# Kernel optimization log

Measured on AMD Instinct MI355X. Metric: run time of the kernel, lower is better.

The kernel has to match this reference:

```python
import jax, jax.numpy as jnp
import numpy as np

B, S, D = 4, 4096, 64

def setup_inputs() -> dict:
    key = jax.random.key(0)
    kq, kk, kv = jax.random.split(key, 3)
    q = jax.random.normal(kq, (B, S, D), dtype=jnp.float32)
    k = jax.random.normal(kk, (B, S, D), dtype=jnp.float32)
    v = jax.random.normal(kv, (B, S, D), dtype=jnp.float32)
    return {"q": q, "k": k, "v": v}

def reference(q, k, v):
    # unnormalized attention: scores [b,i,j], then weighted sum over j
    attn = jnp.einsum('bid,bjd->bij', q, k)
    out = jnp.einsum('bij,bjd->bid', attn, v)
    return out
```

## Files before the change

kernel.cpp:

```cpp
#include <hip/hip_runtime.h>
#include <hip/hip_bf16.h>


#define BATCH 4
#define SEQ   4096
#define DIM   64
#define NCH   64
#define CHUNK 64

typedef float f4  __attribute__((ext_vector_type(4)));
typedef short bf16x8 __attribute__((ext_vector_type(8)));
typedef float f32x4  __attribute__((ext_vector_type(4)));

__device__ inline unsigned short f2bf(float f) {
    union { float f; unsigned u; } v; v.f = f;
    unsigned r = (v.u + 0x7fffu + ((v.u >> 16) & 1u)) >> 16;
    return (unsigned short)r;
}

__global__ __launch_bounds__(256) void k1_partial(const float* __restrict__ K,
                                                  const float* __restrict__ V,
                                                  float* __restrict__ part) {
    __shared__ f4 Ks[1024];
    __shared__ f4 Vs[1024];
    const int bx = blockIdx.x;
    const int t  = threadIdx.x;
    const f4* Kg = (const f4*)(K + (size_t)bx * (CHUNK * DIM));
    const f4* Vg = (const f4*)(V + (size_t)bx * (CHUNK * DIM));
#pragma unroll
    for (int i = 0; i < 4; ++i) {
        Ks[t + 256 * i] = Kg[t + 256 * i];
        Vs[t + 256 * i] = Vg[t + 256 * i];
    }
    __syncthreads();
    const int rg = t >> 4;
    const int cg = t & 15;
    f4 acc0 = 0.f, acc1 = 0.f, acc2 = 0.f, acc3 = 0.f;
#pragma unroll 8
    for (int j = 0; j < CHUNK; ++j) {
        f4 a = Ks[j * 16 + rg];
        f4 v = Vs[j * 16 + cg];
        acc0 += v * a.x;
        acc1 += v * a.y;
        acc2 += v * a.z;
        acc3 += v * a.w;
    }
    f4* P = (f4*)part + (size_t)bx * 1024;
    P[(rg * 4 + 0) * 16 + cg] = acc0;
    P[(rg * 4 + 1) * 16 + cg] = acc1;
    P[(rg * 4 + 2) * 16 + cg] = acc2;
    P[(rg * 4 + 3) * 16 + cg] = acc3;
}

__global__ __launch_bounds__(256) void k2_reduce(const float* __restrict__ part,
                                                 unsigned short* __restrict__ MB) {
    const int tg = blockIdx.x * 256 + threadIdx.x;
    const int b = tg >> 12;
    const int e = tg & 4095;
    float s = 0.f;
#pragma unroll 8
    for (int p = 0; p < NCH; ++p)
        s += part[((size_t)(b * NCH + p)) * 4096 + e];
    const int dp = e >> 6;
    const int c  = e & 63;
    const int ct = c >> 4, m = c & 15;
    const int ks = dp >> 5, quad = (dp >> 3) & 3, j = dp & 7;
    const int idx = (((b * 8 + ct * 2 + ks) * 64) + quad * 16 + m) * 8 + j;
    MB[idx] = f2bf(s);
}

__global__ __launch_bounds__(256) void k3_qm(const float* __restrict__ Q,
                                             const unsigned short* __restrict__ MB,
                                             float* __restrict__ out) {
    const int bx = blockIdx.x;
    const int t  = threadIdx.x;
    const int wave = t >> 6, lane = t & 63;
    const int m = lane & 15, quad = lane >> 4;
    const int b = bx >> 6;
    const int row0 = (bx & 63) * 64 + wave * 16;

    const float* qrow = Q + ((size_t)b * SEQ + row0 + m) * DIM;
    bf16x8 afrag[2];
#pragma unroll
    for (int ks = 0; ks < 2; ++ks) {
        const f4* qp = (const f4*)(qrow + ks * 32 + quad * 8);
        f4 q1 = qp[0], q2 = qp[1];
        bf16x8 a;
        a[0] = (short)f2bf(q1.x); a[1] = (short)f2bf(q1.y);
        a[2] = (short)f2bf(q1.z); a[3] = (short)f2bf(q1.w);
        a[4] = (short)f2bf(q2.x); a[5] = (short)f2bf(q2.y);
        a[6] = (short)f2bf(q2.z); a[7] = (short)f2bf(q2.w);
        afrag[ks] = a;
    }

    const bf16x8* MBv = (const bf16x8*)MB + (size_t)b * 8 * 64;
    f32x4 acc[4];
#pragma unroll
    for (int ct = 0; ct < 4; ++ct) { acc[ct] = (f32x4)0.f; }
#pragma unroll
    for (int ct = 0; ct < 4; ++ct) {
#pragma unroll
        for (int ks = 0; ks < 2; ++ks) {
            bf16x8 bfrag = MBv[(ct * 2 + ks) * 64 + lane];
            acc[ct] = __builtin_amdgcn_mfma_f32_16x16x32_bf16(afrag[ks], bfrag, acc[ct], 0, 0, 0);
        }
    }

    float* orow = out + ((size_t)b * SEQ + row0) * DIM;
#pragma unroll
    for (int ct = 0; ct < 4; ++ct) {
#pragma unroll
        for (int r = 0; r < 4; ++r) {
            orow[(quad * 4 + r) * DIM + ct * 16 + m] = acc[ct][r];
        }
    }
}

extern "C" void kernel_launch(void* const* d_in, const int* in_sizes, int n_in,
                              void* d_out, int out_size, void* d_ws, size_t ws_size,
                              hipStream_t stream) {
    const float* q = (const float*)d_in[0];
    const float* k = (const float*)d_in[1];
    const float* v = (const float*)d_in[2];
    float* out = (float*)d_out;

    float* part = (float*)d_ws;
    unsigned short* MB = (unsigned short*)((char*)d_ws + (size_t)4 * 1024 * 1024);

    k1_partial<<<BATCH * NCH, 256, 0, stream>>>(k, v, part);
    k2_reduce<<<64, 256, 0, stream>>>(part, MB);
    k3_qm<<<BATCH * NCH, 256, 0, stream>>>(q, MB, out);
}
```

Baseline: 74.46 us.

## Fuse three kernels into one cooperative kernel with grid-wide syncs

Replaces the three separate launches (partial K^T V, reduction, Q·M MFMA) with a single cooperative kernel that uses grid.sync between stages. This is meant to remove two kernel launch gaps and their drain/fill overhead. In exchange it adds the cost of two grid-wide barriers and threadfences, and it relies on the 256 blocks being co-resident for the cooperative launch to succeed.

```diff
diff --git a/kernel.cpp b/kernel.cpp
--- a/kernel.cpp
+++ b/kernel.cpp
@@ -1,12 +1,15 @@
 #include <hip/hip_runtime.h>
 #include <hip/hip_bf16.h>
+#include <hip/hip_cooperative_groups.h>
+
+namespace cg = cooperative_groups;
 
 
 #define BATCH 4
 #define SEQ   4096
 #define DIM   64
+#define CHUNK 64
 #define NCH   64
-#define CHUNK 64
 
 typedef float f4  __attribute__((ext_vector_type(4)));
 typedef short bf16x8 __attribute__((ext_vector_type(8)));
@@ -18,101 +21,103 @@
     return (unsigned short)r;
 }
 
-__global__ __launch_bounds__(256) void k1_partial(const float* __restrict__ K,
-                                                  const float* __restrict__ V,
-                                                  float* __restrict__ part) {
+__global__ __launch_bounds__(256) void kfused(const float* __restrict__ Q,
+                                              const float* __restrict__ K,
+                                              const float* __restrict__ V,
+                                              float* __restrict__ out,
+                                              float* __restrict__ part,
+                                              unsigned short* __restrict__ MB) {
+    cg::grid_group grid = cg::this_grid();
     __shared__ f4 Ks[1024];
     __shared__ f4 Vs[1024];
     const int bx = blockIdx.x;
     const int t  = threadIdx.x;
-    const f4* Kg = (const f4*)(K + (size_t)bx * (CHUNK * DIM));
-    const f4* Vg = (const f4*)(V + (size_t)bx * (CHUNK * DIM));
+
+    {
+        const f4* Kg = (const f4*)(K + (size_t)bx * (CHUNK * DIM));
+        const f4* Vg = (const f4*)(V + (size_t)bx * (CHUNK * DIM));
 #pragma unroll
-    for (int i = 0; i < 4; ++i) {
-        Ks[t + 256 * i] = Kg[t + 256 * i];
-        Vs[t + 256 * i] = Vg[t + 256 * i];
+        for (int i = 0; i < 4; ++i) {
+            Ks[t + 256 * i] = Kg[t + 256 * i];
+            Vs[t + 256 * i] = Vg[t + 256 * i];
+        }
+        __syncthreads();
+        const int rg = t >> 4;
+        const int cg_ = t & 15;
+        f4 a0 = 0.f, a1 = 0.f, a2 = 0.f, a3 = 0.f;
+#pragma unroll 8
+        for (int j = 0; j < CHUNK; ++j) {
+            f4 a = Ks[j * 16 + rg];
+            f4 v = Vs[j * 16 + cg_];
+            a0 += v * a.x;
+            a1 += v * a.y;
+            a2 += v * a.z;
+            a3 += v * a.w;
+        }
+        f4* P = (f4*)part + (size_t)bx * 1024;
+        P[(rg * 4 + 0) * 16 + cg_] = a0;
+        P[(rg * 4 + 1) * 16 + cg_] = a1;
+        P[(rg * 4 + 2) * 16 + cg_] = a2;
+        P[(rg * 4 + 3) * 16 + cg_] = a3;
     }
-    __syncthreads();
-    const int rg = t >> 4;
-    const int cg = t & 15;
-    f4 acc0 = 0.f, acc1 = 0.f, acc2 = 0.f, acc3 = 0.f;
+    __threadfence();
+    grid.sync();
+
+    if (bx < 64) {
+        const int tg = bx * 256 + t;
+        const int b = tg >> 12;
+        const int e = tg & 4095;
+        float s = 0.f;
 #pragma unroll 8
-    for (int j = 0; j < CHUNK; ++j) {
-        f4 a = Ks[j * 16 + rg];
-        f4 v = Vs[j * 16 + cg];
-        acc0 += v * a.x;
-        acc1 += v * a.y;
-        acc2 += v * a.z;
-        acc3 += v * a.w;
+        for (int p = 0; p < NCH; ++p)
+            s += part[((size_t)(b * NCH + p)) * 4096 + e];
+        const int dp = e >> 6;
+        const int c  = e & 63;
+        const int ct = c >> 4, m = c & 15;
+        const int ks = dp >> 5, quad = (dp >> 3) & 3, j = dp & 7;
+        MB[(((b * 8 + ct * 2 + ks) * 64) + quad * 16 + m) * 8 + j] = f2bf(s);
     }
-    f4* P = (f4*)part + (size_t)bx * 1024;
-    P[(rg * 4 + 0) * 16 + cg] = acc0;
-    P[(rg * 4 + 1) * 16 + cg] = acc1;
-    P[(rg * 4 + 2) * 16 + cg] = acc2;
-    P[(rg * 4 + 3) * 16 + cg] = acc3;
-}
+    __threadfence();
+    grid.sync();
 
-__global__ __launch_bounds__(256) void k2_reduce(const float* __restrict__ part,
-                                                 unsigned short* __restrict__ MB) {
-    const int tg = blockIdx.x * 256 + threadIdx.x;
-    const int b = tg >> 12;
-    const int e = tg & 4095;
-    float s = 0.f;
-#pragma unroll 8
-    for (int p = 0; p < NCH; ++p)
-        s += part[((size_t)(b * NCH + p)) * 4096 + e];
-    const int dp = e >> 6;
-    const int c  = e & 63;
-    const int ct = c >> 4, m = c & 15;
-    const int ks = dp >> 5, quad = (dp >> 3) & 3, j = dp & 7;
-    const int idx = (((b * 8 + ct * 2 + ks) * 64) + quad * 16 + m) * 8 + j;
-    MB[idx] = f2bf(s);
-}
+    {
+        const int wave = t >> 6, lane = t & 63;
+        const int m = lane & 15, quad = lane >> 4;
+        const int b = bx >> 6;
+        const int row0 = (bx & 63) * 64 + wave * 16;
 
-__global__ __launch_bounds__(256) void k3_qm(const float* __restrict__ Q,
-                                             const unsigned short* __restrict__ MB,
-                                             float* __restrict__ out) {
-    const int bx = blockIdx.x;
-    const int t  = threadIdx.x;
-    const int wave = t >> 6, lane = t & 63;
-    const int m = lane & 15, quad = lane >> 4;
-    const int b = bx >> 6;
-    const int row0 = (bx & 63) * 64 + wave * 16;
-
-    const float* qrow = Q + ((size_t)b * SEQ + row0 + m) * DIM;
-    bf16x8 afrag[2];
-#pragma unroll
-    for (int ks = 0; ks < 2; ++ks) {
-        const f4* qp = (const f4*)(qrow + ks * 32 + quad * 8);
-        f4 q1 = qp[0], q2 = qp[1];
-        bf16x8 a;
-        a[0] = (short)f2bf(q1.x); a[1] = (short)f2bf(q1.y);
-        a[2] = (short)f2bf(q1.z); a[3] = (short)f2bf(q1.w);
-        a[4] = (short)f2bf(q2.x); a[5] = (short)f2bf(q2.y);
-        a[6] = (short)f2bf(q2.z); a[7] = (short)f2bf(q2.w);
-        afrag[ks] = a;
-    }
-
-    const bf16x8* MBv = (const bf16x8*)MB + (size_t)b * 8 * 64;
-    f32x4 acc[4];
-#pragma unroll
-    for (int ct = 0; ct < 4; ++ct) { acc[ct] = (f32x4)0.f; }
-#pragma unroll
-    for (int ct = 0; ct < 4; ++ct) {
+        const float* qrow = Q + ((size_t)b * SEQ + row0 + m) * DIM;
+        bf16x8 afrag[2];
 #pragma unroll
         for (int ks = 0; ks < 2; ++ks) {
-            bf16x8 bfrag = MBv[(ct * 2 + ks) * 64 + lane];
-            acc[ct] = __builtin_amdgcn_mfma_f32_16x16x32_bf16(afrag[ks], bfrag, acc[ct], 0, 0, 0);
+            const f4* qp = (const f4*)(qrow + ks * 32 + quad * 8);
+            f4 q1 = qp[0], q2 = qp[1];
+            bf16x8 a;
+            a[0] = (short)f2bf(q1.x); a[1] = (short)f2bf(q1.y);
+            a[2] = (short)f2bf(q1.z); a[3] = (short)f2bf(q1.w);
+            a[4] = (short)f2bf(q2.x); a[5] = (short)f2bf(q2.y);
+            a[6] = (short)f2bf(q2.z); a[7] = (short)f2bf(q2.w);
+            afrag[ks] = a;
         }
-    }
 
-    float* orow = out + ((size_t)b * SEQ + row0) * DIM;
+        const bf16x8* MBv = (const bf16x8*)MB + (size_t)b * 8 * 64;
+        f32x4 acc[4];
 #pragma unroll
-    for (int ct = 0; ct < 4; ++ct) {
+        for (int ct = 0; ct < 4; ++ct) acc[ct] = (f32x4)0.f;
 #pragma unroll
-        for (int r = 0; r < 4; ++r) {
-            orow[(quad * 4 + r) * DIM + ct * 16 + m] = acc[ct][r];
-        }
+        for (int ct = 0; ct < 4; ++ct)
+#pragma unroll
+            for (int ks = 0; ks < 2; ++ks) {
+                bf16x8 bfrag = MBv[(ct * 2 + ks) * 64 + lane];
+                acc[ct] = __builtin_amdgcn_mfma_f32_16x16x32_bf16(afrag[ks], bfrag, acc[ct], 0, 0, 0);
+            }
+
+        float* orow = out + ((size_t)b * SEQ + row0) * DIM;
+#pragma unroll
+        for (int ct = 0; ct < 4; ++ct)
+#pragma unroll
+            for (int r = 0; r < 4; ++r)
+                orow[(quad * 4 + r) * DIM + ct * 16 + m] = acc[ct][r];
     }
 }
 
@@ -123,11 +128,10 @@
     const float* k = (const float*)d_in[1];
     const float* v = (const float*)d_in[2];
     float* out = (float*)d_out;
-
     float* part = (float*)d_ws;
     unsigned short* MB = (unsigned short*)((char*)d_ws + (size_t)4 * 1024 * 1024);
 
-    k1_partial<<<BATCH * NCH, 256, 0, stream>>>(k, v, part);
-    k2_reduce<<<64, 256, 0, stream>>>(part, MB);
-    k3_qm<<<BATCH * NCH, 256, 0, stream>>>(q, MB, out);
+    void* args[] = { (void*)&q, (void*)&k, (void*)&v, (void*)&out, (void*)&part, (void*)&MB };
+    hipLaunchCooperativeKernel((const void*)kfused, dim3(BATCH * NCH), dim3(256),
+                               args, 0, stream);
 }
```

Result: slower. 182.9 us (+145.7%).
